# Kernel tuning notes

Measured on AMD Instinct MI355X. Metric: run time of the kernel, lower is better.

Reference implementation:

```python
import jax, jax.numpy as jnp
import numpy as np

H = W = M = 16          # 3D token grid
N = H * W * M           # 4096 tokens
D = 256                 # dims == out_dim == key/value dim == x1_dim
HC = 8                  # head_count
D2 = 2 * D              # concat width
C2 = 4 * D              # MixFFN hidden
OUT = D                 # out_dim
UP = OUT // 2           # PatchExpand output channels
B = 4


def _ln(x, g, b, eps=1e-5):
    m = jnp.mean(x, axis=-1, keepdims=True)
    v = jnp.mean(jnp.square(x - m), axis=-1, keepdims=True)
    return (x - m) / jnp.sqrt(v + eps) * g + b


def setup_inputs() -> dict:
    key = jax.random.key(0)
    ks = jax.random.split(key, 16)
    s = 0.02
    inp = {
        "x1": jax.random.normal(ks[0], (B, N, D), jnp.float32),
        "x2": jax.random.normal(ks[1], (B, N, D), jnp.float32),
        # x1_linear (x1_dim -> out_dim)
        "w_x1": s * jax.random.normal(ks[2], (D, OUT), jnp.float32),
        "b_x1": jnp.zeros((OUT,), jnp.float32),
        # CrossAttentionBlock.norm1 (shared for x1 and x2)
        "g_n1": jnp.ones((D,), jnp.float32),
        "be_n1": jnp.zeros((D,), jnp.float32),
        # Cross_Attention.reprojection: 1x1x1 Conv3d D -> 2D == channel matmul
        "w_rep": s * jax.random.normal(ks[3], (D, D2), jnp.float32),
        "b_rep": jnp.zeros((D2,), jnp.float32),
        # Cross_Attention.norm (LayerNorm 2D)
        "g_an": jnp.ones((D2,), jnp.float32),
        "be_an": jnp.zeros((D2,), jnp.float32),
        # CrossAttentionBlock.norm2 (LayerNorm 2D)
        "g_n2": jnp.ones((D2,), jnp.float32),
        "be_n2": jnp.zeros((D2,), jnp.float32),
        # MixFFN_skip fc1 (2D -> 4D), depthwise conv3d, norm1, fc2
        "w_fc1": s * jax.random.normal(ks[4], (D2, C2), jnp.float32),
        "b_fc1": jnp.zeros((C2,), jnp.float32),
        "w_dw": s * jax.random.normal(ks[5], (C2, 1, 3, 3, 3), jnp.float32),
        "b_dw": jnp.zeros((C2,), jnp.float32),
        "g_m1": jnp.ones((C2,), jnp.float32),
        "be_m1": jnp.zeros((C2,), jnp.float32),
        "w_fc2": s * jax.random.normal(ks[6], (C2, D2), jnp.float32),
        "b_fc2": jnp.zeros((D2,), jnp.float32),
        # concat_linear (2*dims -> out_dim)
        "w_cat": s * jax.random.normal(ks[7], (D2, OUT), jnp.float32),
        "b_cat": jnp.zeros((OUT,), jnp.float32),
        # PatchExpand: expand (out_dim -> 4*out_dim, no bias) + LayerNorm(out_dim//2)
        "w_exp": s * jax.random.normal(ks[8], (OUT, 4 * OUT), jnp.float32),
        "g_up": jnp.ones((UP,), jnp.float32),
        "be_up": jnp.zeros((UP,), jnp.float32),
    }
    return inp


def reference(x1, x2, w_x1, b_x1, g_n1, be_n1, w_rep, b_rep, g_an, be_an,
              g_n2, be_n2, w_fc1, b_fc1, w_dw, b_dw, g_m1, be_m1,
              w_fc2, b_fc2, w_cat, b_cat, w_exp, g_up, be_up):
    b = x1.shape[0]
    hk = D // HC  # head key channels (== head value channels here)

    # x1_linear
    x1e = x1 @ w_x1 + b_x1                                 # [B,N,D]

    # shared norm1 applied to both streams
    n1 = _ln(x1e, g_n1, be_n1)
    n2 = _ln(x2, g_n1, be_n1)

    # Cross_Attention (efficient attention, softmax-normalized K/Q)
    kq = jnp.transpose(n2, (0, 2, 1)).reshape(b, HC, hk, N)   # keys==queries
    val = jnp.transpose(n1, (0, 2, 1)).reshape(b, HC, hk, N)
    k = jax.nn.softmax(kq, axis=3)          # softmax over tokens
    q = jax.nn.softmax(kq, axis=2)          # softmax over head channels
    ctx = jnp.einsum('bhkn,bhvn->bhkv', k, val)        # [B,HC,hk,hv]
    att = jnp.einsum('bhkv,bhkn->bhvn', ctx, q)        # [B,HC,hv,N]
    att = att.reshape(b, D, N)                          # concat heads
    # 1x1x1 Conv3d reprojection D -> 2D, then to [B,N,2D] + LayerNorm
    rep = jnp.einsum('bdn,de->bne', att, w_rep) + b_rep
    rep = _ln(rep, g_an, be_an)                         # [B,N,2D]

    # residual concat + attention
    tx = jnp.concatenate([x1e, x2], axis=2) + rep       # [B,N,2D]

    # MixFFN_skip
    h = _ln(tx, g_n2, be_n2) @ w_fc1 + b_fc1            # [B,N,C2]
    hv = jnp.transpose(h, (0, 2, 1)).reshape(b, C2, H, W, M)
    dw = jax.lax.conv_general_dilated(
        hv, w_dw, window_strides=(1, 1, 1), padding='SAME',
        feature_group_count=C2,
        dimension_numbers=('NCDHW', 'OIDHW', 'NCDHW'))
    dw = dw + b_dw[None, :, None, None, None]
    dw = jnp.transpose(dw.reshape(b, C2, N), (0, 2, 1))  # [B,N,C2]
    ax = jax.nn.gelu(_ln(dw + h, g_m1, be_m1), approximate=False)
    mx = tx + (ax @ w_fc2 + b_fc2)                       # [B,N,2D]

    # concat_linear
    y = mx @ w_cat + b_cat                               # [B,N,OUT]

    ye = y @ w_exp                                       # [B,N,4*OUT]
    ye = ye.reshape(b, 8 * N, UP)                        # view+reshape of contiguous
    out = _ln(ye, g_up, be_up)                           # [B,8N,OUT//2]
    return out
```

## Files before the change

### kernel.cpp

```cpp
#include <hip/hip_runtime.h>
#include <math.h>

using u16 = unsigned short;
typedef __bf16 bf16x8 __attribute__((ext_vector_type(8)));
typedef float f32x4 __attribute__((ext_vector_type(4)));

#define BB 4
#define NN 4096
#define DD 256
#define DD2 512
#define CC2 1024
static constexpr int ROWS = BB * NN;
static constexpr size_t MB = 1024 * 1024;

__device__ __forceinline__ u16 f2bf(float f) {
  union { float f; unsigned u; } v; v.f = f;
  unsigned r = v.u + 0x7fffu + ((v.u >> 16) & 1u);
  return (u16)(r >> 16);
}
__device__ __forceinline__ float bf2f(u16 u) {
  union { unsigned u; float f; } v; v.u = ((unsigned)u) << 16;
  return v.f;
}
__device__ __forceinline__ float u2f(unsigned x) {
  union { unsigned u; float f; } v; v.u = x; return v.f;
}
__device__ __forceinline__ void gload16(const void* g, void* l) {
  __builtin_amdgcn_global_load_lds(
      (const __attribute__((address_space(1))) void*)g,
      (__attribute__((address_space(3))) void*)l, 16, 0, 0);
}

__global__ __launch_bounds__(256) void wprep_all(
    const float* __restrict__ w_x1, const float* __restrict__ w_rep,
    const float* __restrict__ w_fc1, const float* __restrict__ w_fc2,
    const float* __restrict__ w_cat, const float* __restrict__ w_exp,
    const float* __restrict__ w_dw,
    u16* __restrict__ w_x1t, u16* __restrict__ w_rept,
    u16* __restrict__ w_fc1t, u16* __restrict__ w_fc2t,
    u16* __restrict__ w_catt, u16* __restrict__ w_expt,
    float* __restrict__ w_dwt) {
  int i = blockIdx.x * 256 + threadIdx.x;
  if (i < 65536) { int n = i >> 8, k = i & 255; w_x1t[i] = f2bf(w_x1[k * 256 + n]); return; }
  i -= 65536;
  if (i < 131072) { int n = i >> 8, k = i & 255; w_rept[i] = f2bf(w_rep[k * 512 + n]); return; }
  i -= 131072;
  if (i < 524288) { int n = i >> 9, k = i & 511; w_fc1t[i] = f2bf(w_fc1[k * 1024 + n]); return; }
  i -= 524288;
  if (i < 524288) { int n = i >> 10, k = i & 1023; w_fc2t[i] = f2bf(w_fc2[k * 512 + n]); return; }
  i -= 524288;
  if (i < 131072) { int n = i >> 9, k = i & 511; w_catt[i] = f2bf(w_cat[k * 256 + n]); return; }
  i -= 131072;
  if (i < 262144) { int n = i >> 8, k = i & 255; w_expt[i] = f2bf(w_exp[k * 1024 + n]); return; }
  i -= 262144;
  if (i < 27648) { int widx = i >> 10, c = i & 1023; w_dwt[i] = w_dw[c * 27 + widx]; }
}

template <int K, int EPI, bool AF32 = false>
__global__ __launch_bounds__(256, 2) void gemm_mfma(
    const u16* __restrict__ A, const u16* __restrict__ Bt,
    const float* __restrict__ bias, const u16* __restrict__ resid,
    void* __restrict__ Cout, int nTilesN,
    const float* __restrict__ gup, const float* __restrict__ beup) {
  const int t = threadIdx.x;
  const int m0 = (blockIdx.x / nTilesN) * 128;
  const int n0 = (blockIdx.x % nTilesN) * 128;
  const int Ncols = nTilesN * 128;
  const int lane = t & 63, wid = t >> 6;
  const int wr = wid >> 1, wc = wid & 1;
  const int lrow = lane & 15, kgrp = lane >> 4;

  __shared__ u16 ldsA[2][128 * 32];
  __shared__ u16 ldsB[2][128 * 32];

  int srow[2], sslot[2];
#pragma unroll
  for (int c = 0; c < 2; ++c) {
    int idx = c * 256 + t;
    srow[c] = idx >> 2;
    sslot[c] = (idx & 3) ^ ((srow[c] >> 1) & 3);
  }

  int offA[4], offB[4];
#pragma unroll
  for (int m = 0; m < 4; ++m) {
    int r = wr * 64 + m * 16 + lrow;
    offA[m] = r * 32 + ((kgrp ^ ((r >> 1) & 3)) * 8);
  }
#pragma unroll
  for (int n = 0; n < 4; ++n) {
    int r = wc * 64 + n * 16 + lrow;
    offB[n] = r * 32 + ((kgrp ^ ((r >> 1) & 3)) * 8);
  }

  f32x4 acc[4][4];
#pragma unroll
  for (int m = 0; m < 4; ++m)
#pragma unroll
    for (int n = 0; n < 4; ++n) acc[m][n] = f32x4{0.f, 0.f, 0.f, 0.f};

  auto loadA32 = [&](int c, int kc) -> uint4 {
    const float* A32 = (const float*)A;
    const float* p = A32 + (size_t)(m0 + srow[c]) * K + kc + sslot[c] * 8;
    float4 f0 = *(const float4*)p;
    float4 f1 = *(const float4*)(p + 4);
    u16 o[8] = {f2bf(f0.x), f2bf(f0.y), f2bf(f0.z), f2bf(f0.w),
                f2bf(f1.x), f2bf(f1.y), f2bf(f1.z), f2bf(f1.w)};
    return *(uint4*)o;
  };
  auto stage_async = [&](int buf, int kc) {
#pragma unroll
    for (int c = 0; c < 2; ++c) {
      gload16(A + (size_t)(m0 + srow[c]) * K + kc + sslot[c] * 8,
              &ldsA[buf][(c * 256 + t) * 8]);
      gload16(Bt + (size_t)(n0 + srow[c]) * K + kc + sslot[c] * 8,
              &ldsB[buf][(c * 256 + t) * 8]);
    }
  };

  uint4 ra[2], rb[2];
  if constexpr (AF32) {
#pragma unroll
    for (int c = 0; c < 2; ++c) {
      ra[c] = loadA32(c, 0);
      rb[c] = *(const uint4*)(Bt + (size_t)(n0 + srow[c]) * K + sslot[c] * 8);
    }
#pragma unroll
    for (int c = 0; c < 2; ++c) {
      int idx = c * 256 + t;
      *(uint4*)&ldsA[0][idx * 8] = ra[c];
      *(uint4*)&ldsB[0][idx * 8] = rb[c];
    }
  } else {
    stage_async(0, 0);
  }
  __syncthreads();

  const int nt = K / 32;
  for (int tt = 0; tt < nt; ++tt) {
    const int cur = tt & 1;
    if (tt + 1 < nt) {
      const int kc = (tt + 1) * 32;
      if constexpr (AF32) {
#pragma unroll
        for (int c = 0; c < 2; ++c) {
          ra[c] = loadA32(c, kc);
          rb[c] = *(const uint4*)(Bt + (size_t)(n0 + srow[c]) * K + kc + sslot[c] * 8);
        }
      } else {
        stage_async(cur ^ 1, kc);
      }
    }
    bf16x8 af[4], bf[4];
#pragma unroll
    for (int m = 0; m < 4; ++m) af[m] = *(const bf16x8*)&ldsA[cur][offA[m]];
#pragma unroll
    for (int n = 0; n < 4; ++n) bf[n] = *(const bf16x8*)&ldsB[cur][offB[n]];
#pragma unroll
    for (int m = 0; m < 4; ++m)
#pragma unroll
      for (int n = 0; n < 4; ++n)
        acc[m][n] = __builtin_amdgcn_mfma_f32_16x16x32_bf16(af[m], bf[n], acc[m][n], 0, 0, 0);
    if (AF32 && tt + 1 < nt) {
#pragma unroll
      for (int c = 0; c < 2; ++c) {
        int idx = c * 256 + t;
        *(uint4*)&ldsA[cur ^ 1][idx * 8] = ra[c];
        *(uint4*)&ldsB[cur ^ 1][idx * 8] = rb[c];
      }
    }
    __syncthreads();
  }

  if (EPI == 3) {
    __shared__ float lnS[2][128], lnQ[2][128];
    float s_[4][4], q_[4][4];
#pragma unroll
    for (int m = 0; m < 4; ++m)
#pragma unroll
      for (int j = 0; j < 4; ++j) {
        float s = 0.f, q = 0.f;
#pragma unroll
        for (int n = 0; n < 4; ++n) {
          float v = acc[m][n][j];
          s += v; q += v * v;
        }
        s_[m][j] = s; q_[m][j] = q;
      }
#pragma unroll
    for (int msk = 1; msk < 16; msk <<= 1) {
#pragma unroll
      for (int m = 0; m < 4; ++m)
#pragma unroll
        for (int j = 0; j < 4; ++j) {
          s_[m][j] += __shfl_xor(s_[m][j], msk, 64);
          q_[m][j] += __shfl_xor(q_[m][j], msk, 64);
        }
    }
    if (lrow == 0) {
#pragma unroll
      for (int m = 0; m < 4; ++m)
#pragma unroll
        for (int j = 0; j < 4; ++j) {
          int r = wr * 64 + m * 16 + kgrp * 4 + j;
          lnS[wc][r] = s_[m][j];
          lnQ[wc][r] = q_[m][j];
        }
    }
    __syncthreads();
#pragma unroll
    for (int m = 0; m < 4; ++m) {
      const int rb0 = wr * 64 + m * 16 + kgrp * 4;
#pragma unroll
      for (int j = 0; j < 4; ++j) {
        const int r = rb0 + j;
        float S = lnS[0][r] + lnS[1][r];
        float Q = lnQ[0][r] + lnQ[1][r];
        float mean = S * (1.0f / 128.0f);
        float var = Q * (1.0f / 128.0f) - mean * mean;
        float iv = rsqrtf(var + 1e-5f);
#pragma unroll
        for (int n = 0; n < 4; ++n) {
          int lc = wc * 64 + n * 16 + lrow;
          ((float*)Cout)[(size_t)(m0 + r) * Ncols + n0 + lc] =
              (acc[m][n][j] - mean) * iv * gup[lc] + beup[lc];
        }
      }
    }
    return;
  }

  float bcol[4];
#pragma unroll
  for (int n = 0; n < 4; ++n) {
    int col = n0 + wc * 64 + n * 16 + (lane & 15);
    bcol[n] = bias ? bias[col] : 0.f;
  }
#pragma unroll
  for (int m = 0; m < 4; ++m) {
    const int r0 = m0 + wr * 64 + m * 16 + kgrp * 4;
#pragma unroll
    for (int n = 0; n < 4; ++n) {
      const int col = n0 + wc * 64 + n * 16 + (lane & 15);
#pragma unroll
      for (int j = 0; j < 4; ++j) {
        float v = acc[m][n][j] + bcol[n];
        size_t idx = (size_t)(r0 + j) * Ncols + col;
        if (EPI == 0) {
          ((float*)Cout)[idx] = v;
        } else if (EPI == 1) {
          ((u16*)Cout)[idx] = f2bf(v);
        } else {
          v += bf2f(resid[idx]);
          ((u16*)Cout)[idx] = f2bf(v);
        }
      }
    }
  }
}

__global__ __launch_bounds__(256) void ln256_both(
    const u16* __restrict__ x1e_b, const float* __restrict__ x2,
    const float* __restrict__ g, const float* __restrict__ be,
    u16* __restrict__ n1T, u16* __restrict__ n2b, u16* __restrict__ n2T) {
  int row = blockIdx.x;
  const int t = threadIdx.x;
  const bool first = row < ROWS;
  if (!first) row -= ROWS;
  __shared__ float ws[8];
  float v = first ? bf2f(x1e_b[(size_t)row * DD + t])
                  : x2[(size_t)row * DD + t];
  float s = v, q = v * v;
#pragma unroll
  for (int m = 1; m < 64; m <<= 1) {
    s += __shfl_xor(s, m, 64);
    q += __shfl_xor(q, m, 64);
  }
  if ((t & 63) == 0) { ws[t >> 6] = s; ws[4 + (t >> 6)] = q; }
  __syncthreads();
  s = ws[0] + ws[1] + ws[2] + ws[3];
  q = ws[4] + ws[5] + ws[6] + ws[7];
  float mean = s * (1.0f / DD);
  float var = q * (1.0f / DD) - mean * mean;
  float iv = rsqrtf(var + 1e-5f);
  u16 rb = f2bf((v - mean) * iv * g[t] + be[t]);
  int b = row >> 12, n = row & 4095;
  if (first) {
    n1T[((size_t)(b * 256 + t)) * 4096 + n] = rb;
  } else {
    n2b[(size_t)row * DD + t] = rb;
    n2T[((size_t)(b * 256 + t)) * 4096 + n] = rb;
  }
}

__global__ __launch_bounds__(256) void k34_ctx(
    const u16* __restrict__ n2T, const u16* __restrict__ n1T,
    float* __restrict__ ctx) {
  const int bid = blockIdx.x;
  const int bx = (bid & 7) * 128 + (bid >> 3);
  const int b = bx >> 8, d = bx & 255;
  const int h = d >> 5, kk = d & 31;
  const int t = threadIdx.x;
  __shared__ u16 prow[4096];
  __shared__ float xred[8];
  __shared__ float sw[128];
  const u16* src = n2T + (size_t)bx * 4096;
  ((uint4*)prow)[t] = ((const uint4*)src)[t];
  ((uint4*)prow)[256 + t] = ((const uint4*)src)[256 + t];
  __syncthreads();
  float mx = -1e30f;
#pragma unroll
  for (int i = 0; i < 16; ++i) mx = fmaxf(mx, bf2f(prow[i * 256 + t]));
#pragma unroll
  for (int m = 1; m < 64; m <<= 1) mx = fmaxf(mx, __shfl_xor(mx, m, 64));
  if ((t & 63) == 0) xred[t >> 6] = mx;
  __syncthreads();
  mx = fmaxf(fmaxf(xred[0], xred[1]), fmaxf(xred[2], xred[3]));
  float sme = 0.f;
#pragma unroll
  for (int i = 0; i < 16; ++i) sme += __expf(bf2f(prow[i * 256 + t]) - mx);
#pragma unroll
  for (int m = 1; m < 64; m <<= 1) sme += __shfl_xor(sme, m, 64);
  if ((t & 63) == 0) xred[4 + (t >> 6)] = sme;
  __syncthreads();
  const float inv = 1.0f / (xred[4] + xred[5] + xred[6] + xred[7]);

  float acc[32];
#pragma unroll
  for (int v = 0; v < 32; ++v) acc[v] = 0.f;
  const u16* vbase = n1T + ((size_t)(b * 256 + h * 32)) * 4096;
  for (int i = 0; i < 16; ++i) {
    const int n = i * 256 + t;
    const float p = __expf(bf2f(prow[n]) - mx) * inv;
#pragma unroll
    for (int v = 0; v < 32; ++v)
      acc[v] += p * bf2f(vbase[(size_t)v * 4096 + n]);
  }
#pragma unroll
  for (int v = 0; v < 32; ++v) {
#pragma unroll
    for (int m = 1; m < 64; m <<= 1) acc[v] += __shfl_xor(acc[v], m, 64);
  }
  if ((t & 63) == 0) {
#pragma unroll
    for (int v = 0; v < 32; ++v) sw[(t >> 6) * 32 + v] = acc[v];
  }
  __syncthreads();
  if (t < 32)
    ctx[(((size_t)(b * 8 + h)) * 32 + kk) * 32 + t] =
        sw[t] + sw[32 + t] + sw[64 + t] + sw[96 + t];
}

__global__ __launch_bounds__(256) void k5_attT(
    const u16* __restrict__ n2, const float* __restrict__ ctx,
    u16* __restrict__ attT) {
  const int row = blockIdx.x, t = threadIdx.x;
  const int b = row >> 12;
  const int h = t >> 5, v = t & 31;
  __shared__ float nr[DD];
  __shared__ float q[DD];
  nr[t] = bf2f(n2[(size_t)row * DD + t]);
  __syncthreads();
  float mx = -1e30f;
  for (int c = 0; c < 32; ++c) mx = fmaxf(mx, nr[h * 32 + c]);
  float sm = 0.f;
  for (int c = 0; c < 32; ++c) sm += __expf(nr[h * 32 + c] - mx);
  q[t] = __expf(nr[t] - mx) / sm;
  __syncthreads();
  const float* cb = ctx + ((size_t)(b * 8 + h) * 32) * 32 + v;
  float acc = 0.f;
#pragma unroll
  for (int k = 0; k < 32; ++k) acc += cb[k * 32] * q[h * 32 + k];
  attT[(size_t)row * DD + t] = f2bf(acc);
}

__global__ __launch_bounds__(256) void l3_reptx(
    const u16* __restrict__ rep_b, const u16* __restrict__ x1e,
    const float* __restrict__ x2,
    const float* __restrict__ g_an, const float* __restrict__ be_an,
    const float* __restrict__ g_n2, const float* __restrict__ be_n2,
    u16* __restrict__ tx, u16* __restrict__ txln) {
  const int row = blockIdx.x, t = threadIdx.x;
  __shared__ float ws[8];
  float a0 = bf2f(rep_b[(size_t)row * DD2 + t]);
  float a1 = bf2f(rep_b[(size_t)row * DD2 + 256 + t]);
  float s = a0 + a1, q = a0 * a0 + a1 * a1;
#pragma unroll
  for (int m = 1; m < 64; m <<= 1) {
    s += __shfl_xor(s, m, 64);
    q += __shfl_xor(q, m, 64);
  }
  if ((t & 63) == 0) { ws[t >> 6] = s; ws[4 + (t >> 6)] = q; }
  __syncthreads();
  s = ws[0] + ws[1] + ws[2] + ws[3];
  q = ws[4] + ws[5] + ws[6] + ws[7];
  float mean = s * (1.0f / DD2);
  float var = q * (1.0f / DD2) - mean * mean;
  float iv = rsqrtf(var + 1e-5f);
  float r0 = (a0 - mean) * iv * g_an[t] + be_an[t];
  float r1 = (a1 - mean) * iv * g_an[256 + t] + be_an[256 + t];
  float t0 = bf2f(x1e[(size_t)row * DD + t]) + r0;
  float t1 = x2[(size_t)row * DD + t] + r1;
  tx[(size_t)row * DD2 + t] = f2bf(t0);
  tx[(size_t)row * DD2 + 256 + t] = f2bf(t1);
  __syncthreads();
  s = t0 + t1; q = t0 * t0 + t1 * t1;
#pragma unroll
  for (int m = 1; m < 64; m <<= 1) {
    s += __shfl_xor(s, m, 64);
    q += __shfl_xor(q, m, 64);
  }
  if ((t & 63) == 0) { ws[t >> 6] = s; ws[4 + (t >> 6)] = q; }
  __syncthreads();
  s = ws[0] + ws[1] + ws[2] + ws[3];
  q = ws[4] + ws[5] + ws[6] + ws[7];
  mean = s * (1.0f / DD2);
  var = q * (1.0f / DD2) - mean * mean;
  iv = rsqrtf(var + 1e-5f);
  txln[(size_t)row * DD2 + t] = f2bf((t0 - mean) * iv * g_n2[t] + be_n2[t]);
  txln[(size_t)row * DD2 + 256 + t] = f2bf((t1 - mean) * iv * g_n2[256 + t] + be_n2[256 + t]);
}

__global__ __launch_bounds__(1024) void c8a_col(
    const u16* __restrict__ h, const float* __restrict__ w_dwt,
    const float* __restrict__ b_dw, const float* __restrict__ g,
    const float* __restrict__ be, u16* __restrict__ ax) {
  const int bid = blockIdx.x;
  const int cidx = (bid & 7) * 128 + (bid >> 3);
  const int b = cidx >> 8, y = (cidx >> 4) & 15, x = cidx & 15;
  const int t = threadIdx.x;
  const int lane = t & 63, wave = t >> 6;
  const size_t hb = (size_t)b * NN * CC2;

  __shared__ float2 red[16][16];
  __shared__ float2 stats[16];

  int coln[9];
  float cmask[9];
#pragma unroll
  for (int dy = -1; dy <= 1; ++dy)
#pragma unroll
    for (int dx = -1; dx <= 1; ++dx) {
      int qq = (dy + 1) * 3 + (dx + 1);
      int yy = y + dy, xx = x + dx;
      bool ok = ((unsigned)yy < 16u) && ((unsigned)xx < 16u);
      coln[qq] = ((ok ? yy : y) << 4) | (ok ? xx : x);
      cmask[qq] = ok ? 1.f : 0.f;
    }

  float wr[3][9];
#pragma unroll
  for (int p = 0; p < 3; ++p)
#pragma unroll
    for (int qq = 0; qq < 9; ++qq)
      wr[p][qq] = w_dwt[(p * 9 + qq) * CC2 + t] * cmask[qq];
  const float bias = b_dw[t];

  u16 win[3][9];
#define LOADPLANE(ZL, SLOT)                                                   \
  do {                                                                        \
    if ((ZL) >= 0 && (ZL) < 16) {                                             \
      _Pragma("unroll") for (int qq = 0; qq < 9; ++qq) win[SLOT][qq] =        \
          h[hb + (size_t)((((ZL) << 8) | coln[qq])) * CC2 + t];               \
    } else {                                                                  \
      _Pragma("unroll") for (int qq = 0; qq < 9; ++qq) win[SLOT][qq] = 0;     \
    }                                                                         \
  } while (0)

  LOADPLANE(-1, 0);
  LOADPLANE(0, 1);
  LOADPLANE(1, 2);

  float vs[16];
#pragma unroll
  for (int z = 0; z < 16; ++z) {
    const int pm1 = z % 3, pz = (z + 1) % 3, pp1 = (z + 2) % 3;
    float a0 = bias;
#pragma unroll
    for (int qq = 0; qq < 9; ++qq) {
      a0 += bf2f(win[pm1][qq]) * wr[0][qq];
      a0 += bf2f(win[pz][qq]) * wr[1][qq];
      a0 += bf2f(win[pp1][qq]) * wr[2][qq];
    }
    float v = a0 + bf2f(win[pz][4]);
    LOADPLANE(z + 2, pm1);
    vs[z] = v;
    float s = v, q2 = v * v;
#pragma unroll
    for (int m = 1; m < 64; m <<= 1) {
      s += __shfl_xor(s, m, 64);
      q2 += __shfl_xor(q2, m, 64);
    }
    if (lane == 0) red[z][wave] = make_float2(s, q2);
  }
#undef LOADPLANE
  __syncthreads();

  {
    const int z = wave;
    float S = (lane < 16) ? red[z][lane].x : 0.f;
    float Q = (lane < 16) ? red[z][lane].y : 0.f;
#pragma unroll
    for (int m = 1; m < 16; m <<= 1) {
      S += __shfl_xor(S, m, 64);
      Q += __shfl_xor(Q, m, 64);
    }
    if (lane == 0) {
      float mean = S * (1.0f / CC2);
      float var = Q * (1.0f / CC2) - mean * mean;
      stats[z] = make_float2(mean, rsqrtf(var + 1e-5f));
    }
  }
  __syncthreads();

  const float gg = g[t], bb = be[t];
#pragma unroll
  for (int z = 0; z < 16; ++z) {
    float2 st = stats[z];
    float u = (vs[z] - st.x) * st.y * gg + bb;
    float s2 = 1.5957691216f * (u + 0.044715f * u * u * u);
    float o = u / (1.0f + __expf(-s2));
    ax[((size_t)(b * NN + ((z << 8) | (y << 4) | x))) * CC2 + t] = f2bf(o);
  }
}

extern "C" void kernel_launch(void* const* d_in, const int* in_sizes, int n_in,
                              void* d_out, int out_size, void* d_ws, size_t ws_size,
                              hipStream_t stream) {
  const float* x1    = (const float*)d_in[0];
  const float* x2    = (const float*)d_in[1];
  const float* w_x1  = (const float*)d_in[2];
  const float* b_x1  = (const float*)d_in[3];
  const float* g_n1  = (const float*)d_in[4];
  const float* be_n1 = (const float*)d_in[5];
  const float* w_rep = (const float*)d_in[6];
  const float* b_rep = (const float*)d_in[7];
  const float* g_an  = (const float*)d_in[8];
  const float* be_an = (const float*)d_in[9];
  const float* g_n2  = (const float*)d_in[10];
  const float* be_n2 = (const float*)d_in[11];
  const float* w_fc1 = (const float*)d_in[12];
  const float* b_fc1 = (const float*)d_in[13];
  const float* w_dw  = (const float*)d_in[14];
  const float* b_dw  = (const float*)d_in[15];
  const float* g_m1  = (const float*)d_in[16];
  const float* be_m1 = (const float*)d_in[17];
  const float* w_fc2 = (const float*)d_in[18];
  const float* b_fc2 = (const float*)d_in[19];
  const float* w_cat = (const float*)d_in[20];
  const float* b_cat = (const float*)d_in[21];
  const float* w_exp = (const float*)d_in[22];
  const float* g_up  = (const float*)d_in[23];
  const float* be_up = (const float*)d_in[24];

  char* ws = (char*)d_ws;
  float* out = (float*)d_out;

  u16*   x1e_b   = (u16*)(ws + 8 * MB);
  u16*   n1T     = (u16*)(ws + 24 * MB);
  u16*   n2b     = (u16*)(ws + 32 * MB);
  u16*   n2T     = (u16*)(ws + 40 * MB);
  float* ctx     = (float*)(ws + 48 * MB);
  u16*   rep_b   = (u16*)(ws + 49 * MB);
  u16*   tx      = (u16*)(ws + 81 * MB);
  u16*   txln    = (u16*)(ws + 97 * MB);
  u16*   hbuf    = (u16*)(ws + 113 * MB);
  u16*   attT    = (u16*)(ws + 0);
  u16*   ax      = (u16*)(ws + 49 * MB);
  u16*   mx      = (u16*)(ws + 8 * MB);
  u16*   ybuf    = (u16*)(ws + 0);
  u16*   w_x1t   = (u16*)(ws + 145 * MB);
  u16*   w_rept  = w_x1t + 256 * 256;
  u16*   w_fc1t  = w_rept + 512 * 256;
  u16*   w_fc2t  = w_fc1t + 1024 * 512;
  u16*   w_catt  = w_fc2t + 512 * 1024;
  u16*   w_expt  = w_catt + 256 * 512;
  float* w_dwt   = (float*)(ws + 149 * MB);

  wprep_all<<<(1666048 + 255) / 256, 256, 0, stream>>>(
      w_x1, w_rep, w_fc1, w_fc2, w_cat, w_exp, w_dw,
      w_x1t, w_rept, w_fc1t, w_fc2t, w_catt, w_expt, w_dwt);

  gemm_mfma<256, 1, true><<<(ROWS / 128) * 2, 256, 0, stream>>>(
      (const u16*)x1, w_x1t, b_x1, nullptr, x1e_b, 2, nullptr, nullptr);
  ln256_both<<<2 * ROWS, 256, 0, stream>>>(x1e_b, x2, g_n1, be_n1, n1T, n2b, n2T);
  k34_ctx<<<BB * 256, 256, 0, stream>>>(n2T, n1T, ctx);
  k5_attT<<<ROWS, 256, 0, stream>>>(n2b, ctx, attT);
  gemm_mfma<256, 1><<<(ROWS / 128) * 4, 256, 0, stream>>>(
      attT, w_rept, b_rep, nullptr, rep_b, 4, nullptr, nullptr);
  l3_reptx<<<ROWS, 256, 0, stream>>>(rep_b, x1e_b, x2, g_an, be_an, g_n2, be_n2, tx, txln);
  gemm_mfma<512, 1><<<(ROWS / 128) * 8, 256, 0, stream>>>(
      txln, w_fc1t, b_fc1, nullptr, hbuf, 8, nullptr, nullptr);
  c8a_col<<<1024, 1024, 0, stream>>>(hbuf, w_dwt, b_dw, g_m1, be_m1, ax);
  gemm_mfma<1024, 2><<<(ROWS / 128) * 4, 256, 0, stream>>>(
      ax, w_fc2t, b_fc2, tx, mx, 4, nullptr, nullptr);
  gemm_mfma<512, 1><<<(ROWS / 128) * 2, 256, 0, stream>>>(
      mx, w_catt, b_cat, nullptr, ybuf, 2, nullptr, nullptr);
  gemm_mfma<256, 3><<<(ROWS / 128) * 8, 256, 0, stream>>>(
      ybuf, w_expt, nullptr, nullptr, out, 8, g_up, be_up);
}
```

Baseline: 320.3 us.

## Fold concat_linear into PatchExpand and ctx into reprojection weights; swizzle GEMM grid

Precomputes w_cat@w_exp and its combined bias so the concat_linear GEMM disappears and the final LN GEMM runs directly from mx with K=512. It also precomputes per-batch ctx@w_rep matrices, so the attention apply and reprojection collapse into one per-batch GEMM on softmaxed queries. The query softmax is moved into the layernorm kernel, and GEMM block indices are remapped across groups of 8 for cache locality. The final GEMM now does more FLOPs (K doubles over 8 N-tiles versus a separate small GEMM), and bf16 rounding of the combined weights changes numerics slightly.

```diff
diff --git a/kernel.cpp b/kernel.cpp
--- a/kernel.cpp
+++ b/kernel.cpp
@@ -35,11 +35,11 @@
     const float* __restrict__ w_x1, const float* __restrict__ w_rep,
     const float* __restrict__ w_fc1, const float* __restrict__ w_fc2,
     const float* __restrict__ w_cat, const float* __restrict__ w_exp,
-    const float* __restrict__ w_dw,
+    const float* __restrict__ w_dw, const float* __restrict__ b_cat,
     u16* __restrict__ w_x1t, u16* __restrict__ w_rept,
     u16* __restrict__ w_fc1t, u16* __restrict__ w_fc2t,
-    u16* __restrict__ w_catt, u16* __restrict__ w_expt,
-    float* __restrict__ w_dwt) {
+    u16* __restrict__ w_cat_b, u16* __restrict__ w_expt,
+    float* __restrict__ w_dwt, float* __restrict__ b_comb) {
   int i = blockIdx.x * 256 + threadIdx.x;
   if (i < 65536) { int n = i >> 8, k = i & 255; w_x1t[i] = f2bf(w_x1[k * 256 + n]); return; }
   i -= 65536;
@@ -49,23 +49,33 @@
   i -= 524288;
   if (i < 524288) { int n = i >> 10, k = i & 1023; w_fc2t[i] = f2bf(w_fc2[k * 512 + n]); return; }
   i -= 524288;
-  if (i < 131072) { int n = i >> 9, k = i & 511; w_catt[i] = f2bf(w_cat[k * 256 + n]); return; }
+  if (i < 131072) { w_cat_b[i] = f2bf(w_cat[i]); return; }
   i -= 131072;
   if (i < 262144) { int n = i >> 8, k = i & 255; w_expt[i] = f2bf(w_exp[k * 1024 + n]); return; }
   i -= 262144;
-  if (i < 27648) { int widx = i >> 10, c = i & 1023; w_dwt[i] = w_dw[c * 27 + widx]; }
-}
-
-template <int K, int EPI, bool AF32 = false>
+  if (i < 27648) { int widx = i >> 10, c = i & 1023; w_dwt[i] = w_dw[c * 27 + widx]; return; }
+  i -= 27648;
+  if (i < 1024) {
+    float acc = 0.f;
+    for (int o = 0; o < 256; ++o) acc += b_cat[o] * w_exp[o * 1024 + i];
+    b_comb[i] = acc;
+  }
+}
+
+template <int K, int EPI, bool AF32 = false, bool PERB = false>
 __global__ __launch_bounds__(256, 2) void gemm_mfma(
     const u16* __restrict__ A, const u16* __restrict__ Bt,
     const float* __restrict__ bias, const u16* __restrict__ resid,
     void* __restrict__ Cout, int nTilesN,
     const float* __restrict__ gup, const float* __restrict__ beup) {
   const int t = threadIdx.x;
-  const int m0 = (blockIdx.x / nTilesN) * 128;
-  const int n0 = (blockIdx.x % nTilesN) * 128;
+  int bid = blockIdx.x;
+  const int nwg = gridDim.x;
+  if ((nwg & 7) == 0) bid = (bid & 7) * (nwg >> 3) + (bid >> 3);
+  const int m0 = (bid / nTilesN) * 128;
+  const int n0 = (bid % nTilesN) * 128;
   const int Ncols = nTilesN * 128;
+  if (PERB) Bt += (size_t)(m0 >> 12) * (size_t)Ncols * K;
   const int lane = t & 63, wid = t >> 6;
   const int wr = wid >> 1, wc = wid & 1;
   const int lrow = lane & 15, kgrp = lane >> 4;
@@ -173,6 +183,12 @@
   }
 
   if (EPI == 3) {
+    float bcol3[4];
+#pragma unroll
+    for (int n = 0; n < 4; ++n) {
+      int gc = n0 + wc * 64 + n * 16 + lrow;
+      bcol3[n] = bias ? bias[gc] : 0.f;
+    }
     __shared__ float lnS[2][128], lnQ[2][128];
     float s_[4][4], q_[4][4];
 #pragma unroll
@@ -182,7 +198,7 @@
         float s = 0.f, q = 0.f;
 #pragma unroll
         for (int n = 0; n < 4; ++n) {
-          float v = acc[m][n][j];
+          float v = acc[m][n][j] + bcol3[n];
           s += v; q += v * v;
         }
         s_[m][j] = s; q_[m][j] = q;
@@ -223,7 +239,7 @@
         for (int n = 0; n < 4; ++n) {
           int lc = wc * 64 + n * 16 + lrow;
           ((float*)Cout)[(size_t)(m0 + r) * Ncols + n0 + lc] =
-              (acc[m][n][j] - mean) * iv * gup[lc] + beup[lc];
+              (acc[m][n][j] + bcol3[n] - mean) * iv * gup[lc] + beup[lc];
         }
       }
     }
@@ -262,7 +278,7 @@
 __global__ __launch_bounds__(256) void ln256_both(
     const u16* __restrict__ x1e_b, const float* __restrict__ x2,
     const float* __restrict__ g, const float* __restrict__ be,
-    u16* __restrict__ n1T, u16* __restrict__ n2b, u16* __restrict__ n2T) {
+    u16* __restrict__ n1T, u16* __restrict__ n2T, u16* __restrict__ qmat) {
   int row = blockIdx.x;
   const int t = threadIdx.x;
   const bool first = row < ROWS;
@@ -288,8 +304,16 @@
   if (first) {
     n1T[((size_t)(b * 256 + t)) * 4096 + n] = rb;
   } else {
-    n2b[(size_t)row * DD + t] = rb;
     n2T[((size_t)(b * 256 + t)) * 4096 + n] = rb;
+    float vq = bf2f(rb);
+    float hm = vq;
+#pragma unroll
+    for (int m = 1; m < 32; m <<= 1) hm = fmaxf(hm, __shfl_xor(hm, m, 32));
+    float he = __expf(vq - hm);
+    float hs = he;
+#pragma unroll
+    for (int m = 1; m < 32; m <<= 1) hs += __shfl_xor(hs, m, 32);
+    qmat[(size_t)row * DD + t] = f2bf(he / hs);
   }
 }
 
@@ -351,27 +375,38 @@
         sw[t] + sw[32 + t] + sw[64 + t] + sw[96 + t];
 }
 
-__global__ __launch_bounds__(256) void k5_attT(
-    const u16* __restrict__ n2, const float* __restrict__ ctx,
-    u16* __restrict__ attT) {
-  const int row = blockIdx.x, t = threadIdx.x;
-  const int b = row >> 12;
-  const int h = t >> 5, v = t & 31;
-  __shared__ float nr[DD];
-  __shared__ float q[DD];
-  nr[t] = bf2f(n2[(size_t)row * DD + t]);
-  __syncthreads();
-  float mx = -1e30f;
-  for (int c = 0; c < 32; ++c) mx = fmaxf(mx, nr[h * 32 + c]);
-  float sm = 0.f;
-  for (int c = 0; c < 32; ++c) sm += __expf(nr[h * 32 + c] - mx);
-  q[t] = __expf(nr[t] - mx) / sm;
-  __syncthreads();
-  const float* cb = ctx + ((size_t)(b * 8 + h) * 32) * 32 + v;
-  float acc = 0.f;
-#pragma unroll
-  for (int k = 0; k < 32; ++k) acc += cb[k * 32] * q[h * 32 + k];
-  attT[(size_t)row * DD + t] = f2bf(acc);
+__global__ __launch_bounds__(256) void m2_build(
+    const float* __restrict__ ctx, const u16* __restrict__ w_rept,
+    u16* __restrict__ m2t) {
+  const int b = blockIdx.x >> 4, ec = blockIdx.x & 15;
+  const int t = threadIdx.x;
+  const int e = ec * 32 + (t >> 3), h = t & 7;
+  __shared__ float cl[8192];
+#pragma unroll
+  for (int i = 0; i < 8; ++i)
+    *(float4*)(cl + t * 32 + i * 4) = *(const float4*)(ctx + b * 8192 + t * 32 + i * 4);
+  __syncthreads();
+  float wf[32];
+  {
+    u16 wv[32];
+#pragma unroll
+    for (int i = 0; i < 4; ++i)
+      *(uint4*)(wv + i * 8) = *(const uint4*)(w_rept + (size_t)e * 256 + h * 32 + i * 8);
+#pragma unroll
+    for (int v = 0; v < 32; ++v) wf[v] = bf2f(wv[v]);
+  }
+  u16 outv[32];
+#pragma unroll
+  for (int kk = 0; kk < 32; ++kk) {
+    float acc = 0.f;
+    const float* cp = cl + h * 1024 + kk * 32;
+#pragma unroll
+    for (int v = 0; v < 32; ++v) acc += cp[v] * wf[v];
+    outv[kk] = f2bf(acc);
+  }
+  u16* dst = m2t + ((size_t)(b * 512 + e)) * 256 + h * 32;
+#pragma unroll
+  for (int i = 0; i < 4; ++i) *(uint4*)(dst + i * 8) = *(uint4*)(outv + i * 8);
 }
 
 __global__ __launch_bounds__(256) void l3_reptx(
@@ -556,46 +591,48 @@
   char* ws = (char*)d_ws;
   float* out = (float*)d_out;
 
+  u16*   qmat    = (u16*)(ws + 0);
   u16*   x1e_b   = (u16*)(ws + 8 * MB);
   u16*   n1T     = (u16*)(ws + 24 * MB);
-  u16*   n2b     = (u16*)(ws + 32 * MB);
   u16*   n2T     = (u16*)(ws + 40 * MB);
   float* ctx     = (float*)(ws + 48 * MB);
   u16*   rep_b   = (u16*)(ws + 49 * MB);
   u16*   tx      = (u16*)(ws + 81 * MB);
   u16*   txln    = (u16*)(ws + 97 * MB);
   u16*   hbuf    = (u16*)(ws + 113 * MB);
-  u16*   attT    = (u16*)(ws + 0);
   u16*   ax      = (u16*)(ws + 49 * MB);
   u16*   mx      = (u16*)(ws + 8 * MB);
-  u16*   ybuf    = (u16*)(ws + 0);
   u16*   w_x1t   = (u16*)(ws + 145 * MB);
   u16*   w_rept  = w_x1t + 256 * 256;
   u16*   w_fc1t  = w_rept + 512 * 256;
   u16*   w_fc2t  = w_fc1t + 1024 * 512;
-  u16*   w_catt  = w_fc2t + 512 * 1024;
-  u16*   w_expt  = w_catt + 256 * 512;
+  u16*   w_cat_b = w_fc2t + 512 * 1024;
+  u16*   w_expt  = w_cat_b + 512 * 256;
   float* w_dwt   = (float*)(ws + 149 * MB);
-
-  wprep_all<<<(1666048 + 255) / 256, 256, 0, stream>>>(
-      w_x1, w_rep, w_fc1, w_fc2, w_cat, w_exp, w_dw,
-      w_x1t, w_rept, w_fc1t, w_fc2t, w_catt, w_expt, w_dwt);
+  u16*   w_combT = (u16*)(ws + 150 * MB);
+  float* b_comb  = (float*)(ws + 151 * MB);
+  u16*   m2t     = (u16*)(ws + 152 * MB);
+
+  wprep_all<<<(1667072 + 255) / 256, 256, 0, stream>>>(
+      w_x1, w_rep, w_fc1, w_fc2, w_cat, w_exp, w_dw, b_cat,
+      w_x1t, w_rept, w_fc1t, w_fc2t, w_cat_b, w_expt, w_dwt, b_comb);
+
+  gemm_mfma<256, 1><<<32, 256, 0, stream>>>(
+      w_expt, w_cat_b, nullptr, nullptr, w_combT, 4, nullptr, nullptr);
 
   gemm_mfma<256, 1, true><<<(ROWS / 128) * 2, 256, 0, stream>>>(
       (const u16*)x1, w_x1t, b_x1, nullptr, x1e_b, 2, nullptr, nullptr);
-  ln256_both<<<2 * ROWS, 256, 0, stream>>>(x1e_b, x2, g_n1, be_n1, n1T, n2b, n2T);
+  ln256_both<<<2 * ROWS, 256, 0, stream>>>(x1e_b, x2, g_n1, be_n1, n1T, n2T, qmat);
   k34_ctx<<<BB * 256, 256, 0, stream>>>(n2T, n1T, ctx);
-  k5_attT<<<ROWS, 256, 0, stream>>>(n2b, ctx, attT);
-  gemm_mfma<256, 1><<<(ROWS / 128) * 4, 256, 0, stream>>>(
-      attT, w_rept, b_rep, nullptr, rep_b, 4, nullptr, nullptr);
+  m2_build<<<64, 256, 0, stream>>>(ctx, w_rept, m2t);
+  gemm_mfma<256, 1, false, true><<<(ROWS / 128) * 4, 256, 0, stream>>>(
+      qmat, m2t, b_rep, nullptr, rep_b, 4, nullptr, nullptr);
   l3_reptx<<<ROWS, 256, 0, stream>>>(rep_b, x1e_b, x2, g_an, be_an, g_n2, be_n2, tx, txln);
   gemm_mfma<512, 1><<<(ROWS / 128) * 8, 256, 0, stream>>>(
       txln, w_fc1t, b_fc1, nullptr, hbuf, 8, nullptr, nullptr);
   c8a_col<<<1024, 1024, 0, stream>>>(hbuf, w_dwt, b_dw, g_m1, be_m1, ax);
   gemm_mfma<1024, 2><<<(ROWS / 128) * 4, 256, 0, stream>>>(
       ax, w_fc2t, b_fc2, tx, mx, 4, nullptr, nullptr);
-  gemm_mfma<512, 1><<<(ROWS / 128) * 2, 256, 0, stream>>>(
-      mx, w_catt, b_cat, nullptr, ybuf, 2, nullptr, nullptr);
-  gemm_mfma<256, 3><<<(ROWS / 128) * 8, 256, 0, stream>>>(
-      ybuf, w_expt, nullptr, nullptr, out, 8, g_up, be_up);
-}
+  gemm_mfma<512, 3><<<(ROWS / 128) * 8, 256, 0, stream>>>(
+      mx, w_combT, b_comb, nullptr, out, 8, g_up, be_up);
+}
```

After: 327.9 us. 2.4% more time.
